# Optimization experiments

Hardware: AMD Instinct MI355X
Metric: run time of the kernel (lower is better)

The kernel has to match this reference:

```python
import jax, jax.numpy as jnp
import numpy as np

B, N = 4, 8192
MODEL_DIM, FEAT, HEADS, DIM, SIZE = 512, 64, 8, 3, 32
BN_EPS = 1e-5


def setup_inputs() -> dict:
    key = jax.random.key(0)
    ks = jax.random.split(key, 8)
    return {
        "input": jax.random.normal(ks[0], (B, MODEL_DIM, N), jnp.float32),
        "orig_pcd": jax.random.uniform(ks[1], (B, 3, N), jnp.float32, minval=-1.0, maxval=1.0),
        "conv_w": jax.random.normal(ks[2], (HEADS * (FEAT + 3), MODEL_DIM), jnp.float32) * (MODEL_DIM ** -0.5),
        "key_gamma": jax.random.normal(ks[3], (HEADS * 3,), jnp.float32) * 0.1,
        "key_beta": jnp.zeros((HEADS * 3,), jnp.float32),
        "val_gamma": jnp.ones((HEADS * FEAT,), jnp.float32),
        "val_beta": jnp.zeros((HEADS * FEAT,), jnp.float32),
        "proj": jax.random.normal(ks[4], (HEADS, DIM, 3), jnp.float32) * 0.5,
    }


def _bn(x, gamma, beta):
    # train-mode BatchNorm1d: normalize each channel over (batch, length); x: [B, C, N]
    mu = jnp.mean(x, axis=(0, 2), keepdims=True)
    var = jnp.var(x, axis=(0, 2), keepdims=True)
    xhat = (x - mu) * jax.lax.rsqrt(var + BN_EPS)
    return xhat * gamma[None, :, None] + beta[None, :, None]


def _splat(lattice, values):
    # lattice: [B, H, DIM, N] in (-1, 1); values: [B, H*FEAT, N]
    # DifferentiablePositions: map (-1,1) -> continuous grid coords in [0, SIZE-1]
    c = (lattice + 1.0) * 0.5 * (SIZE - 1)
    f = jnp.clip(jnp.floor(c), 0, SIZE - 2).astype(jnp.int32)   # base corner
    r = c - f.astype(c.dtype)                                    # local coord, [B,H,DIM,N]
    vals = values.reshape(B, HEADS, FEAT, N)
    data = jnp.moveaxis(vals, 2, -1)                             # [B,H,N,FEAT]
    strides = jnp.array([SIZE ** (DIM - 1 - d) for d in range(DIM)], jnp.int32)
    ncells = SIZE ** DIM
    bh = jnp.arange(B)[:, None] * HEADS + jnp.arange(HEADS)[None, :]  # [B,H]
    z = jnp.zeros((B * HEADS * ncells, FEAT), jnp.float32)
    # trilinear splat: scatter-add into the 2^DIM surrounding lattice cells
    for corner in range(2 ** DIM):
        bits = jnp.array([(corner >> (DIM - 1 - d)) & 1 for d in range(DIM)], jnp.int32)
        bits4 = bits[None, None, :, None]
        idx = f + bits4                                           # [B,H,DIM,N]
        w = jnp.prod(jnp.where(bits4 == 1, r, 1.0 - r), axis=2)   # [B,H,N]
        flat = jnp.sum(idx * strides[None, None, :, None], axis=2)  # [B,H,N]
        gid = (bh[:, :, None] * ncells + flat).reshape(-1)        # [B*H*N]
        z = z.at[gid].add((data * w[..., None]).reshape(-1, FEAT))
    return z.reshape(B, HEADS, ncells, FEAT).transpose(0, 1, 3, 2).reshape((B, HEADS, FEAT) + (SIZE,) * DIM)


def reference(input, orig_pcd, conv_w, key_gamma, key_beta, val_gamma, val_beta, proj):
    # 1x1 conv == channel GEMM: [B, H*(FEAT+3), N]
    kv = jnp.einsum('om,bmn->bon', conv_w, input)
    keys_res = _bn(kv[:, :HEADS * 3], key_gamma, key_beta)        # [B, H*3, N]
    values = _bn(kv[:, HEADS * 3:], val_gamma, val_beta)          # [B, H*FEAT, N]
    # per-head learned 3D->DIM projection of (pcd + predicted offset)
    pts = orig_pcd[:, None] + keys_res.reshape(B, HEADS, 3, N)    # [B,H,3,N]
    keys = jnp.einsum('hdk,bhkn->bhdn', proj, pts)                # [B,H,DIM,N]
    lattice = jnp.tanh(keys)
    z = _splat(lattice, values)                                   # [B,H,FEAT,S,S,S]
    occ = (jnp.abs(z) > 1e-9).sum().astype(jnp.float32) / (B * FEAT * HEADS)
    return z, occ, jnp.mean(keys), jnp.var(keys)
```

## Files before the change

kernel.cpp:

```cpp
#include <hip/hip_runtime.h>

#define B_     4
#define N_     8192
#define MD_    512
#define OC_    536
#define HEADS_ 8
#define FEAT_  64
#define NC_    32768
#define ZTOT_  67108864ll
#define NPTS_  262144
#define NKEYS_ 786432.0f
#define BNINV_ (1.0f / 32768.0f)

typedef __bf16 bf16x8 __attribute__((ext_vector_type(8)));
typedef float  f32x4  __attribute__((ext_vector_type(4)));

__device__ __forceinline__ unsigned short f2bf(float f) {
  unsigned int u = __float_as_uint(f);
  u = (u + 0x7FFFu + ((u >> 16) & 1u)) >> 16;
  return (unsigned short)u;
}
__device__ __forceinline__ float bf2f(unsigned short s) {
  return __uint_as_float(((unsigned)s) << 16);
}

__global__ __launch_bounds__(256) void convw_kernel(const float* __restrict__ W,
                                                    unsigned short* __restrict__ Wbf) {
  int i = (blockIdx.x * 256 + threadIdx.x) * 4;
  float4 v = *(const float4*)&W[24 * 512 + i];
  ushort4 o;
  o.x = f2bf(v.x); o.y = f2bf(v.y); o.z = f2bf(v.z); o.w = f2bf(v.w);
  *(ushort4*)&Wbf[i] = o;
}

__global__ __launch_bounds__(256) void convxt_kernel(const float* __restrict__ X,
                                                     unsigned short* __restrict__ Xt) {
  const int n0 = blockIdx.x * 64;
  const int k0 = blockIdx.y * 64;
  const int b  = blockIdx.z;
  __shared__ float T[64][65];
  const int t = threadIdx.x;
#pragma unroll
  for (int i = 0; i < 16; ++i) {
    int idx = t + i * 256;
    int kk = idx >> 6, nn = idx & 63;
    T[kk][nn] = X[((size_t)b * MD_ + k0 + kk) * N_ + n0 + nn];
  }
  __syncthreads();
  const int sub = t & 7;
  const int nb  = t >> 3;
#pragma unroll
  for (int i = 0; i < 2; ++i) {
    int nn = nb + i * 32;
    ushort4 o0, o1;
    o0.x = f2bf(T[sub * 8 + 0][nn]); o0.y = f2bf(T[sub * 8 + 1][nn]);
    o0.z = f2bf(T[sub * 8 + 2][nn]); o0.w = f2bf(T[sub * 8 + 3][nn]);
    o1.x = f2bf(T[sub * 8 + 4][nn]); o1.y = f2bf(T[sub * 8 + 5][nn]);
    o1.z = f2bf(T[sub * 8 + 6][nn]); o1.w = f2bf(T[sub * 8 + 7][nn]);
    unsigned short* dst = Xt + ((size_t)b * N_ + n0 + nn) * MD_ + k0 + sub * 8;
    *(ushort4*)dst = o0;
    *(ushort4*)(dst + 4) = o1;
  }
}

__global__ __launch_bounds__(256) void gemm_mfma(const unsigned short* __restrict__ Wbf,
                                                 const unsigned short* __restrict__ Xt,
                                                 const float* __restrict__ W,
                                                 const float* __restrict__ X,
                                                 unsigned short* __restrict__ valsbf,
                                                 float* __restrict__ kvk,
                                                 float* __restrict__ ssum,
                                                 float* __restrict__ s2sum) {
  __shared__ __align__(16) unsigned short smem[128 * 144];
  const int t = threadIdx.x;
  const int b = blockIdx.z;

  if (blockIdx.y == 4) {
    const int n0 = blockIdx.x * 128;
    float* Wt = (float*)smem;
    float* In = (float*)smem + 32 * 26;
    const int cg = t & 31;
    const int rb = (t >> 5) * 3;
    float acc[3][4];
#pragma unroll
    for (int r = 0; r < 3; ++r)
#pragma unroll
      for (int c = 0; c < 4; ++c) acc[r][c] = 0.f;
    const float* Xb = X + (size_t)b * MD_ * N_;
    for (int k0 = 0; k0 < MD_; k0 += 32) {
#pragma unroll
      for (int i = 0; i < 3; ++i) {
        int idx = t * 3 + i;
        int m = idx % 24, k = idx / 24;
        Wt[k * 26 + m] = W[(size_t)m * MD_ + k0 + k];
      }
#pragma unroll
      for (int i = 0; i < 4; ++i) {
        int slot = t + i * 256;
        int k = slot >> 5, n4 = slot & 31;
        float4 v = *(const float4*)(Xb + (size_t)(k0 + k) * N_ + n0 + n4 * 4);
        *(float4*)&In[k * 132 + n4 * 4] = v;
      }
      __syncthreads();
#pragma unroll
      for (int k = 0; k < 32; ++k) {
        float4 bv = *(const float4*)&In[k * 132 + cg * 4];
#pragma unroll
        for (int r = 0; r < 3; ++r) {
          float a = Wt[k * 26 + rb + r];
          acc[r][0] = fmaf(a, bv.x, acc[r][0]);
          acc[r][1] = fmaf(a, bv.y, acc[r][1]);
          acc[r][2] = fmaf(a, bv.z, acc[r][2]);
          acc[r][3] = fmaf(a, bv.w, acc[r][3]);
        }
      }
      __syncthreads();
    }
#pragma unroll
    for (int r = 0; r < 3; ++r) {
      float* dst = kvk + ((size_t)b * 24 + rb + r) * N_ + n0 + cg * 4;
      *(float4*)dst = *(float4*)&acc[r][0];
      float s = acc[r][0] + acc[r][1] + acc[r][2] + acc[r][3];
      float s2 = acc[r][0]*acc[r][0] + acc[r][1]*acc[r][1] +
                 acc[r][2]*acc[r][2] + acc[r][3]*acc[r][3];
#pragma unroll
      for (int off = 16; off; off >>= 1) {
        s  += __shfl_down(s, off, 32);
        s2 += __shfl_down(s2, off, 32);
      }
      if (cg == 0) { atomicAdd(&ssum[rb + r], s); atomicAdd(&s2sum[rb + r], s2); }
    }
    return;
  }

#define AL(r, c) smem[(r) * 72 + (c)]
#define BL(r, c) smem[128 * 72 + (r) * 72 + (c)]
#define CS(r, c) smem[(r) * 136 + (c)]
  const int n0 = blockIdx.x * 128;
  const int m0 = blockIdx.y * 128;
  const int lane = t & 63, wave = t >> 6;
  const int wm = wave >> 1, wn = wave & 1;
  f32x4 acc[4][4];
#pragma unroll
  for (int mi = 0; mi < 4; ++mi)
#pragma unroll
    for (int ni = 0; ni < 4; ++ni)
#pragma unroll
      for (int j = 0; j < 4; ++j) acc[mi][ni][j] = 0.f;

  const unsigned short* Xb = Xt + ((size_t)b * N_ + n0) * MD_;
  for (int k0 = 0; k0 < MD_; k0 += 64) {
#pragma unroll
    for (int i = 0; i < 4; ++i) {
      int chunk = t + i * 256;
      int r = chunk >> 3, c = chunk & 7;
      *(uint4*)&AL(r, c * 8) =
          *(const uint4*)&Wbf[(size_t)(m0 + r) * MD_ + k0 + c * 8];
    }
#pragma unroll
    for (int i = 0; i < 4; ++i) {
      int chunk = t + i * 256;
      int r = chunk >> 3, c = chunk & 7;
      *(uint4*)&BL(r, c * 8) =
          *(const uint4*)&Xb[(size_t)r * MD_ + k0 + c * 8];
    }
    __syncthreads();
#pragma unroll
    for (int ks = 0; ks < 2; ++ks) {
      bf16x8 af[4], bfr[4];
#pragma unroll
      for (int mi = 0; mi < 4; ++mi)
        af[mi] = *(const bf16x8*)&AL(wm * 64 + mi * 16 + (lane & 15),
                                     ks * 32 + (lane >> 4) * 8);
#pragma unroll
      for (int ni = 0; ni < 4; ++ni)
        bfr[ni] = *(const bf16x8*)&BL(wn * 64 + ni * 16 + (lane & 15),
                                      ks * 32 + (lane >> 4) * 8);
#pragma unroll
      for (int mi = 0; mi < 4; ++mi)
#pragma unroll
        for (int ni = 0; ni < 4; ++ni)
          acc[mi][ni] = __builtin_amdgcn_mfma_f32_16x16x32_bf16(
              af[mi], bfr[ni], acc[mi][ni], 0, 0, 0);
    }
    __syncthreads();
  }
#pragma unroll
  for (int mi = 0; mi < 4; ++mi)
#pragma unroll
    for (int j = 0; j < 4; ++j) {
      float s  = acc[mi][0][j] + acc[mi][1][j] + acc[mi][2][j] + acc[mi][3][j];
      float s2 = acc[mi][0][j]*acc[mi][0][j] + acc[mi][1][j]*acc[mi][1][j] +
                 acc[mi][2][j]*acc[mi][2][j] + acc[mi][3][j]*acc[mi][3][j];
#pragma unroll
      for (int off = 1; off < 16; off <<= 1) {
        s  += __shfl_xor(s, off);
        s2 += __shfl_xor(s2, off);
      }
      if ((lane & 15) == 0) {
        int mg = m0 + wm * 64 + mi * 16 + (lane >> 4) * 4 + j;
        atomicAdd(&ssum[24 + mg], s);
        atomicAdd(&s2sum[24 + mg], s2);
      }
    }
#pragma unroll
  for (int mi = 0; mi < 4; ++mi)
#pragma unroll
    for (int ni = 0; ni < 4; ++ni) {
      int row = wm * 64 + mi * 16 + (lane >> 4) * 4;
      int col = wn * 64 + ni * 16 + (lane & 15);
#pragma unroll
      for (int j = 0; j < 4; ++j)
        CS(row + j, col) = f2bf(acc[mi][ni][j]);
    }
  __syncthreads();
#pragma unroll
  for (int i = 0; i < 4; ++i) {
    int row = (t >> 3) + i * 32;
    int cb  = (t & 7) * 16;
    uint4 lo = *(const uint4*)&CS(row, cb);
    uint4 hi = *(const uint4*)&CS(row, cb + 8);
    unsigned short* dst = valsbf + ((size_t)b * 512 + m0 + row) * N_ + n0 + cb;
    *(uint4*)dst       = lo;
    *(uint4*)(dst + 8) = hi;
  }
#undef AL
#undef BL
#undef CS
}

__global__ __launch_bounds__(1024, 1) void sortk_kernel(const float* __restrict__ kvk,
                                                        const float* __restrict__ orig,
                                                        const float* __restrict__ proj,
                                                        const float* __restrict__ ssum,
                                                        const float* __restrict__ s2sum,
                                                        const float* __restrict__ kg,
                                                        const float* __restrict__ kb,
                                                        float4* __restrict__ sorted,
                                                        float* __restrict__ kacc) {
  const int bh = blockIdx.x;
  const int b = bh >> 3, h = bh & 7;
  __shared__ int hist[NC_];
  __shared__ int wsum[16];
  const int t = threadIdx.x;
  for (int i = t; i < NC_; i += 1024) hist[i] = 0;

  float sck[3], shk[3];
#pragma unroll
  for (int k = 0; k < 3; ++k) {
    int ch = h * 3 + k;
    float mu  = ssum[ch] * BNINV_;
    float var = s2sum[ch] * BNINV_ - mu * mu;
    sck[k] = kg[ch] * rsqrtf(var + 1e-5f);
    shk[k] = kb[ch] - mu * sck[k];
  }
  __syncthreads();

  const float* Kb = kvk + (size_t)b * 24 * N_;
  const float* Ob = orig + (size_t)b * 3 * N_;
  float4 mreg[8];
  float ksum = 0.f, ksq = 0.f;
#pragma unroll
  for (int i = 0; i < 8; ++i) {
    const int n = t + i * 1024;
    float pt[3];
#pragma unroll
    for (int k = 0; k < 3; ++k) {
      float kr = fmaf(Kb[(size_t)(h * 3 + k) * N_ + n], sck[k], shk[k]);
      pt[k] = Ob[(size_t)k * N_ + n] + kr;
    }
    int cell = 0;
    float rr[3];
#pragma unroll
    for (int d = 0; d < 3; ++d) {
      const float* pr = proj + (h * 3 + d) * 3;
      float key = pr[0] * pt[0] + pr[1] * pt[1] + pr[2] * pt[2];
      ksum += key; ksq += key * key;
      float lat = tanhf(key);
      float c = (lat + 1.0f) * 15.5f;
      float fl = floorf(c);
      fl = fminf(fmaxf(fl, 0.0f), 30.0f);
      rr[d] = c - fl;
      cell += (int)fl * ((d == 0) ? 1024 : (d == 1) ? 32 : 1);
    }
    mreg[i] = make_float4(rr[0], rr[1], rr[2], __int_as_float(cell | (n << 15)));
    atomicAdd(&hist[cell], 1);
  }
#pragma unroll
  for (int off = 32; off; off >>= 1) {
    ksum += __shfl_down(ksum, off);
    ksq  += __shfl_down(ksq, off);
  }
  if ((t & 63) == 0) {
    atomicAdd(&kacc[0], ksum);
    atomicAdd(&kacc[1], ksq);
  }
  __syncthreads();

  const int base = t * 32;
  int s = 0;
#pragma unroll
  for (int j = 0; j < 32; ++j) s += hist[base + ((j + t) & 31)];
  const int lane = t & 63, wv = t >> 6;
  int sc = s;
#pragma unroll
  for (int off = 1; off < 64; off <<= 1) {
    int x = __shfl_up(sc, off);
    if (lane >= off) sc += x;
  }
  if (lane == 63) wsum[wv] = sc;
  __syncthreads();
  if (t < 16) {
    int x = wsum[t];
    int sc2 = x;
#pragma unroll
    for (int off = 1; off < 16; off <<= 1) {
      int y = __shfl_up(sc2, off);
      if (t >= off) sc2 += y;
    }
    wsum[t] = sc2 - x;
  }
  __syncthreads();
  int run = sc - s + wsum[wv];
#pragma unroll
  for (int j = 0; j < 32; ++j) {
    int idx = base + ((j + t) & 31);
    int v = hist[idx];
    hist[idx] = run;
    run += v;
  }
  __syncthreads();
  float4* dst = sorted + (size_t)bh * N_;
#pragma unroll
  for (int i = 0; i < 8; ++i) {
    float4 m = mreg[i];
    int cell = __float_as_int(m.w) & 32767;
    int pos = atomicAdd(&hist[cell], 1);
    dst[pos] = m;
  }
}

__global__ __launch_bounds__(512, 1) void accum_kernel(const unsigned short* __restrict__ valsbf,
                                                       const float* __restrict__ ssum,
                                                       const float* __restrict__ s2sum,
                                                       const float* __restrict__ vg,
                                                       const float* __restrict__ vb,
                                                       const float4* __restrict__ sorted,
                                                       float* __restrict__ zout,
                                                       unsigned int* __restrict__ occ) {
  const int blk = blockIdx.x;
  const int f   = blk & 63;
  const int bh  = blk >> 6;
  const int b = bh >> 3, h = bh & 7;
  __shared__ float tile[NC_];
  __shared__ unsigned short kvs[N_];
  const int t = threadIdx.x;
#pragma unroll
  for (int i = 0; i < 16; ++i)
    ((float4*)tile)[t + i * 512] = make_float4(0.f, 0.f, 0.f, 0.f);
  const unsigned short* kvrow = valsbf + ((size_t)b * 512 + h * 64 + f) * N_;
  ((uint4*)kvs)[t]       = ((const uint4*)kvrow)[t];
  ((uint4*)kvs)[t + 512] = ((const uint4*)kvrow)[t + 512];
  __syncthreads();

  const int ch = 24 + h * 64 + f;
  const float mu  = ssum[ch] * BNINV_;
  const float var = s2sum[ch] * BNINV_ - mu * mu;
  const float sc  = vg[ch - 24] * rsqrtf(var + 1e-5f);
  const float sh  = vb[ch - 24] - mu * sc;
  const float4* sp = sorted + (size_t)bh * N_;
  const int base = t * 16;

  float4 e[16];
#pragma unroll
  for (int i = 0; i < 16; ++i) e[i] = sp[base + i];

#define FLUSH8()                                                    \
  {                                                                 \
    atomicAdd(&tile[cur],        m0_);                              \
    atomicAdd(&tile[cur + 1],    m1_);                              \
    atomicAdd(&tile[cur + 32],   m2_);                              \
    atomicAdd(&tile[cur + 33],   m3_);                              \
    atomicAdd(&tile[cur + 1024], m4_);                              \
    atomicAdd(&tile[cur + 1025], m5_);                              \
    atomicAdd(&tile[cur + 1056], m6_);                              \
    atomicAdd(&tile[cur + 1057], m7_);                              \
  }

  float m0_ = 0.f, m1_ = 0.f, m2_ = 0.f, m3_ = 0.f;
  float m4_ = 0.f, m5_ = 0.f, m6_ = 0.f, m7_ = 0.f;
  int cur = __float_as_int(e[0].w) & 32767;
#pragma unroll
  for (int i = 0; i < 16; ++i) {
    int packed = __float_as_int(e[i].w);
    int cell = packed & 32767;
    if (cell != cur) {
      if (cell == cur + 1) {
        atomicAdd(&tile[cur],        m0_);
        atomicAdd(&tile[cur + 32],   m2_);
        atomicAdd(&tile[cur + 1024], m4_);
        atomicAdd(&tile[cur + 1056], m6_);
        m0_ = m1_; m2_ = m3_; m4_ = m5_; m6_ = m7_;
        m1_ = 0.f; m3_ = 0.f; m5_ = 0.f; m7_ = 0.f;
      } else {
        FLUSH8();
        m0_ = m1_ = m2_ = m3_ = m4_ = m5_ = m6_ = m7_ = 0.f;
      }
      cur = cell;
    }
    float v  = fmaf(bf2f(kvs[(unsigned)packed >> 15]), sc, sh);
    float r0 = e[i].x, r1 = e[i].y, r2 = e[i].z;
    float va = v * (1.f - r0), vb2 = v * r0;
    float c00 = (1.f - r1) * (1.f - r2), c01 = (1.f - r1) * r2;
    float c10 = r1 * (1.f - r2),         c11 = r1 * r2;
    m0_ = fmaf(va, c00, m0_); m1_ = fmaf(va, c01, m1_);
    m2_ = fmaf(va, c10, m2_); m3_ = fmaf(va, c11, m3_);
    m4_ = fmaf(vb2, c00, m4_); m5_ = fmaf(vb2, c01, m5_);
    m6_ = fmaf(vb2, c10, m6_); m7_ = fmaf(vb2, c11, m7_);
  }
  FLUSH8();
#undef FLUSH8
  __syncthreads();

  unsigned int cnt = 0;
  float* dst = zout + (size_t)blk * NC_;
#pragma unroll
  for (int i = 0; i < 16; ++i) {
    float4 v = ((const float4*)tile)[t + i * 512];
    cnt += (fabsf(v.x) > 1e-9f) ? 1u : 0u;
    cnt += (fabsf(v.y) > 1e-9f) ? 1u : 0u;
    cnt += (fabsf(v.z) > 1e-9f) ? 1u : 0u;
    cnt += (fabsf(v.w) > 1e-9f) ? 1u : 0u;
    ((float4*)dst)[t + i * 512] = v;
  }
#pragma unroll
  for (int off = 32; off; off >>= 1) cnt += __shfl_down(cnt, off);
  __shared__ unsigned int wc[8];
  if ((t & 63) == 0) wc[t >> 6] = cnt;
  __syncthreads();
  if (t == 0) {
    unsigned int s = 0;
#pragma unroll
    for (int i = 0; i < 8; ++i) s += wc[i];
    atomicAdd(occ, s);
  }
}

__global__ __launch_bounds__(256) void gemm_full_kernel(const float* __restrict__ W,
                                                        const float* __restrict__ X,
                                                        float* __restrict__ KV) {
  const int n0 = blockIdx.x * 256;
  const int m0 = blockIdx.y * 64;
  const int b  = blockIdx.z;
  __shared__ float Wt[32][68];
  __shared__ float In[32][260];
  const int t  = threadIdx.x;
  const int tx = t & 31;
  const int ty = t >> 5;
  float acc[8][8];
#pragma unroll
  for (int r = 0; r < 8; ++r)
#pragma unroll
    for (int c = 0; c < 8; ++c) acc[r][c] = 0.f;
  const float* Xb = X + (size_t)b * MD_ * N_;
  for (int k0 = 0; k0 < MD_; k0 += 32) {
#pragma unroll
    for (int i = 0; i < 8; ++i) {
      int idx = t + i * 256;
      int m = idx >> 5, k = idx & 31;
      int mm = m0 + m;
      Wt[k][m] = (mm < OC_) ? W[(size_t)mm * MD_ + (k0 + k)] : 0.f;
    }
#pragma unroll
    for (int i = 0; i < 8; ++i) {
      int slot = t + i * 256;
      int k = slot >> 6, n4 = slot & 63;
      float4 v = *(const float4*)(Xb + (size_t)(k0 + k) * N_ + n0 + n4 * 4);
      *(float4*)&In[k][n4 * 4] = v;
    }
    __syncthreads();
#pragma unroll
    for (int k = 0; k < 32; ++k) {
      float a[8], bb[8];
      *(float4*)&a[0]  = *(const float4*)&Wt[k][ty * 8];
      *(float4*)&a[4]  = *(const float4*)&Wt[k][ty * 8 + 4];
      *(float4*)&bb[0] = *(const float4*)&In[k][tx * 4];
      *(float4*)&bb[4] = *(const float4*)&In[k][128 + tx * 4];
#pragma unroll
      for (int r = 0; r < 8; ++r)
#pragma unroll
        for (int c = 0; c < 8; ++c)
          acc[r][c] = fmaf(a[r], bb[c], acc[r][c]);
    }
    __syncthreads();
  }
#pragma unroll
  for (int r = 0; r < 8; ++r) {
    int mm = m0 + ty * 8 + r;
    if (mm < OC_) {
      float* dst = KV + ((size_t)b * OC_ + mm) * N_ + n0;
      *(float4*)(dst + tx * 4)       = *(float4*)&acc[r][0];
      *(float4*)(dst + 128 + tx * 4) = *(float4*)&acc[r][4];
    }
  }
}

__global__ __launch_bounds__(256) void bn_kernel(const float* __restrict__ KV,
                                                 const float* __restrict__ kg,
                                                 const float* __restrict__ kb,
                                                 const float* __restrict__ vg,
                                                 const float* __restrict__ vb,
                                                 float* __restrict__ scale,
                                                 float* __restrict__ shift) {
  const int o = blockIdx.x;
  const int t = threadIdx.x;
  float s = 0.f, s2 = 0.f;
  for (int idx = t; idx < B_ * N_; idx += 256) {
    int bb = idx >> 13, n = idx & (N_ - 1);
    float v = KV[((size_t)bb * OC_ + o) * N_ + n];
    s += v; s2 = fmaf(v, v, s2);
  }
#pragma unroll
  for (int off = 32; off; off >>= 1) {
    s  += __shfl_down(s, off);
    s2 += __shfl_down(s2, off);
  }
  __shared__ float rs[4], rs2[4];
  if ((t & 63) == 0) { rs[t >> 6] = s; rs2[t >> 6] = s2; }
  __syncthreads();
  if (t == 0) {
    s  = rs[0] + rs[1] + rs[2] + rs[3];
    s2 = rs2[0] + rs2[1] + rs2[2] + rs2[3];
    const float inv = 1.0f / (B_ * N_);
    float mu  = s * inv;
    float var = s2 * inv - mu * mu;
    float g, be;
    if (o < 24) { g = kg[o]; be = kb[o]; }
    else        { g = vg[o - 24]; be = vb[o - 24]; }
    float sc = g * rsqrtf(var + 1e-5f);
    scale[o] = sc;
    shift[o] = be - mu * sc;
  }
}

__global__ __launch_bounds__(256) void splat_final_kernel(const float* __restrict__ KV,
                                                          const float* __restrict__ orig,
                                                          const float* __restrict__ proj,
                                                          const float* __restrict__ scale,
                                                          const float* __restrict__ shift,
                                                          float* __restrict__ Z,
                                                          float* __restrict__ kacc) {
  const int bh = blockIdx.x >> 7;
  const int n0 = (blockIdx.x & 127) << 6;
  const int b = bh >> 3, h = bh & 7;
  __shared__ float vals[64][65];
  __shared__ int   cellS[64];
  __shared__ float rS[64][4];
  const int t = threadIdx.x;
  const float* KVb = KV + (size_t)b * OC_ * N_;
  const int ch0 = 24 + h * 64;
#pragma unroll
  for (int i = 0; i < 16; ++i) {
    int idx = t + i * 256;
    int f = idx >> 6, p = idx & 63;
    int ch = ch0 + f;
    vals[f][p] = fmaf(KVb[(size_t)ch * N_ + n0 + p], scale[ch], shift[ch]);
  }
  if (t < 64) {
    const int n = n0 + t;
    float pt[3];
#pragma unroll
    for (int k = 0; k < 3; ++k) {
      int ch = h * 3 + k;
      float kr = fmaf(KVb[(size_t)ch * N_ + n], scale[ch], shift[ch]);
      pt[k] = orig[((size_t)b * 3 + k) * N_ + n] + kr;
    }
    float ksum = 0.f, ksq = 0.f;
    int cell = 0;
    float rr[3];
#pragma unroll
    for (int d = 0; d < 3; ++d) {
      const float* pr = proj + (h * 3 + d) * 3;
      float key = pr[0] * pt[0] + pr[1] * pt[1] + pr[2] * pt[2];
      ksum += key; ksq += key * key;
      float lat = tanhf(key);
      float c = (lat + 1.0f) * 15.5f;
      float fl = floorf(c);
      fl = fminf(fmaxf(fl, 0.0f), 30.0f);
      rr[d] = c - fl;
      cell += (int)fl * ((d == 0) ? 1024 : (d == 1) ? 32 : 1);
    }
    cellS[t] = cell;
    rS[t][0] = rr[0]; rS[t][1] = rr[1]; rS[t][2] = rr[2];
#pragma unroll
    for (int off = 32; off; off >>= 1) {
      ksum += __shfl_down(ksum, off);
      ksq  += __shfl_down(ksq, off);
    }
    if (t == 0) { atomicAdd(&kacc[0], ksum); atomicAdd(&kacc[1], ksq); }
  }
  __syncthreads();
  const int w = t >> 6, l = t & 63;
  for (int pi = 0; pi < 16; ++pi) {
    int p = w * 16 + pi;
    int cell = cellS[p];
    float r0 = rS[p][0], r1 = rS[p][1], r2 = rS[p][2];
    float u0 = 1.f - r0, u1 = 1.f - r1, u2 = 1.f - r2;
    float v = vals[l][p];
#pragma unroll
    for (int c = 0; c < 8; ++c) {
      float wt = ((c & 4) ? r0 : u0) * ((c & 2) ? r1 : u1) * ((c & 1) ? r2 : u2);
      int cc = cell + ((c & 4) ? 1024 : 0) + ((c & 2) ? 32 : 0) + (c & 1);
      atomicAdd(Z + (size_t)(bh * 64 + l) * NC_ + cc, v * wt);
    }
  }
}

__global__ __launch_bounds__(256) void count_kernel(const float* __restrict__ Z,
                                                    unsigned int* __restrict__ occ) {
  unsigned int cnt = 0;
  for (long long i = (long long)blockIdx.x * blockDim.x + threadIdx.x; i < ZTOT_;
       i += (long long)gridDim.x * blockDim.x)
    cnt += (fabsf(Z[i]) > 1e-9f) ? 1u : 0u;
#pragma unroll
  for (int off = 32; off; off >>= 1) cnt += __shfl_down(cnt, off);
  __shared__ unsigned int wc[4];
  const int t = threadIdx.x;
  if ((t & 63) == 0) wc[t >> 6] = cnt;
  __syncthreads();
  if (t == 0) atomicAdd(occ, wc[0] + wc[1] + wc[2] + wc[3]);
}

__global__ void finalize_kernel(const unsigned int* __restrict__ occ,
                                const float* __restrict__ kacc,
                                float* __restrict__ tail) {
  float mean = kacc[0] / NKEYS_;
  tail[0] = (float)(*occ) * (1.0f / 2048.0f);
  tail[1] = mean;
  tail[2] = kacc[1] / NKEYS_ - mean * mean;
}

extern "C" void kernel_launch(void* const* d_in, const int* in_sizes, int n_in,
                              void* d_out, int out_size, void* d_ws, size_t ws_size,
                              hipStream_t stream) {
  const float* X    = (const float*)d_in[0];
  const float* orig = (const float*)d_in[1];
  const float* W    = (const float*)d_in[2];
  const float* kg   = (const float*)d_in[3];
  const float* kb   = (const float*)d_in[4];
  const float* vg   = (const float*)d_in[5];
  const float* vb   = (const float*)d_in[6];
  const float* proj = (const float*)d_in[7];
  float* out = (float*)d_out;

  float* P = (float*)d_ws;
  float* ssum  = P;
  float* s2sum = P + 544;
  float* kacc  = P + 1088;
  unsigned int* occ = (unsigned int*)(P + 1090);
  float* scale = P + 1152;
  float* shift = P + 1696;
  char* wsb = (char*)d_ws;

  const size_t need = (size_t)60 << 20;
  if (ws_size >= need) {
    unsigned short* Wbf    = (unsigned short*)(wsb + 65536);
    float*          kvk    = (float*)(wsb + ((size_t)1 << 20));
    float4*         sorted = (float4*)(wsb + ((size_t)5 << 20));
    unsigned short* valsbf = (unsigned short*)(wsb + ((size_t)9 << 20));
    unsigned short* Xt = (unsigned short*)out;

    hipMemsetAsync(P, 0, 4368, stream);

    convw_kernel<<<256, 256, 0, stream>>>(W, Wbf);
    convxt_kernel<<<dim3(128, 8, 4), 256, 0, stream>>>(X, Xt);
    gemm_mfma<<<dim3(64, 5, 4), 256, 0, stream>>>(Wbf, Xt, W, X,
                                                  valsbf, kvk, ssum, s2sum);
    sortk_kernel<<<32, 1024, 0, stream>>>(kvk, orig, proj, ssum, s2sum,
                                          kg, kb, sorted, kacc);
    accum_kernel<<<2048, 512, 0, stream>>>(valsbf, ssum, s2sum, vg, vb,
                                           sorted, out, occ);
    finalize_kernel<<<1, 1, 0, stream>>>(occ, kacc, out + ZTOT_);
  } else {
    float* kv = (float*)(wsb + 16384);
    hipMemsetAsync(P, 0, 4368, stream);
    hipMemsetAsync(out, 0, (size_t)ZTOT_ * 4, stream);
    gemm_full_kernel<<<dim3(N_ / 256, 9, B_), 256, 0, stream>>>(W, X, kv);
    bn_kernel<<<OC_, 256, 0, stream>>>(kv, kg, kb, vg, vb, scale, shift);
    splat_final_kernel<<<B_ * HEADS_ * (N_ / 64), 256, 0, stream>>>(
        kv, orig, proj, scale, shift, out, kacc);
    count_kernel<<<2048, 256, 0, stream>>>(out, occ);
    finalize_kernel<<<1, 1, 0, stream>>>(occ, kacc, out + ZTOT_);
  }
}
```

Baseline: 484.0 us.

## Split accum grid tile into four cell-range quarters to shrink LDS and raise occupancy

The accumulation kernel now splits each (batch, head, feature) grid tile into four quarters along the slowest axis, so each block holds an 8192-float LDS tile instead of 32768 and drops the one-block-per-CU launch bound. The sort kernel records, per quarter, the range of sorted points whose splats can touch that quarter, and each block walks only that range, clipping atomics to its quarter. The aim is to fit several blocks per CU and hide latency. In exchange, points near quarter borders are read and processed by two blocks, the launch has four times as many blocks, and the variable-length loop with bounds checks adds branching.

```diff
diff --git a/kernel.cpp b/kernel.cpp
--- a/kernel.cpp
+++ b/kernel.cpp
@@ -237,6 +237,8 @@
                                                         const float* __restrict__ kg,
                                                         const float* __restrict__ kb,
                                                         float4* __restrict__ sorted,
+                                                        int* __restrict__ qlo,
+                                                        int* __restrict__ qhi,
                                                         float* __restrict__ kacc) {
   const int bh = blockIdx.x;
   const int b = bh >> 3, h = bh & 7;
@@ -330,6 +332,11 @@
     run += v;
   }
   __syncthreads();
+  if (t < 4) {
+    qlo[bh * 4 + t] = (t == 0) ? 0 : hist[t * 8192 - 1057];
+    qhi[bh * 4 + t] = (t == 3) ? N_ : hist[(t + 1) * 8192];
+  }
+  __syncthreads();
   float4* dst = sorted + (size_t)bh * N_;
 #pragma unroll
   for (int i = 0; i < 8; ++i) {
@@ -340,23 +347,26 @@
   }
 }
 
-__global__ __launch_bounds__(512, 1) void accum_kernel(const unsigned short* __restrict__ valsbf,
-                                                       const float* __restrict__ ssum,
-                                                       const float* __restrict__ s2sum,
-                                                       const float* __restrict__ vg,
-                                                       const float* __restrict__ vb,
-                                                       const float4* __restrict__ sorted,
-                                                       float* __restrict__ zout,
-                                                       unsigned int* __restrict__ occ) {
+__global__ __launch_bounds__(512) void accum_kernel(const unsigned short* __restrict__ valsbf,
+                                                    const float* __restrict__ ssum,
+                                                    const float* __restrict__ s2sum,
+                                                    const float* __restrict__ vg,
+                                                    const float* __restrict__ vb,
+                                                    const float4* __restrict__ sorted,
+                                                    const int* __restrict__ qlo,
+                                                    const int* __restrict__ qhi,
+                                                    float* __restrict__ zout,
+                                                    unsigned int* __restrict__ occ) {
   const int blk = blockIdx.x;
-  const int f   = blk & 63;
-  const int bh  = blk >> 6;
+  const int q   = blk & 3;
+  const int f   = (blk >> 2) & 63;
+  const int bh  = blk >> 8;
   const int b = bh >> 3, h = bh & 7;
-  __shared__ float tile[NC_];
+  __shared__ float tile[8192];
   __shared__ unsigned short kvs[N_];
   const int t = threadIdx.x;
 #pragma unroll
-  for (int i = 0; i < 16; ++i)
+  for (int i = 0; i < 4; ++i)
     ((float4*)tile)[t + i * 512] = make_float4(0.f, 0.f, 0.f, 0.f);
   const unsigned short* kvrow = valsbf + ((size_t)b * 512 + h * 64 + f) * N_;
   ((uint4*)kvs)[t]       = ((const uint4*)kvrow)[t];
@@ -369,63 +379,78 @@
   const float sc  = vg[ch - 24] * rsqrtf(var + 1e-5f);
   const float sh  = vb[ch - 24] - mu * sc;
   const float4* sp = sorted + (size_t)bh * N_;
-  const int base = t * 16;
-
-  float4 e[16];
-#pragma unroll
-  for (int i = 0; i < 16; ++i) e[i] = sp[base + i];
-
-#define FLUSH8()                                                    \
-  {                                                                 \
-    atomicAdd(&tile[cur],        m0_);                              \
-    atomicAdd(&tile[cur + 1],    m1_);                              \
-    atomicAdd(&tile[cur + 32],   m2_);                              \
-    atomicAdd(&tile[cur + 33],   m3_);                              \
-    atomicAdd(&tile[cur + 1024], m4_);                              \
-    atomicAdd(&tile[cur + 1025], m5_);                              \
-    atomicAdd(&tile[cur + 1056], m6_);                              \
-    atomicAdd(&tile[cur + 1057], m7_);                              \
+  const int lo = q << 13;
+
+  const int e_lo = qlo[bh * 4 + q];
+  const int e_hi = qhi[bh * 4 + q];
+  const int count = e_hi - e_lo;
+  const int span = (count + 511) >> 9;
+  const int s0 = e_lo + t * span;
+  const int s1 = min(s0 + span, e_hi);
+
+#define FLUSH8() {                                                             \
+    int i0 = cur - lo;                                                         \
+    if ((unsigned)i0 < 8192u)          atomicAdd(&tile[i0],        m0_);       \
+    if ((unsigned)(i0 + 1) < 8192u)    atomicAdd(&tile[i0 + 1],    m1_);       \
+    if ((unsigned)(i0 + 32) < 8192u)   atomicAdd(&tile[i0 + 32],   m2_);       \
+    if ((unsigned)(i0 + 33) < 8192u)   atomicAdd(&tile[i0 + 33],   m3_);       \
+    if ((unsigned)(i0 + 1024) < 8192u) atomicAdd(&tile[i0 + 1024], m4_);       \
+    if ((unsigned)(i0 + 1025) < 8192u) atomicAdd(&tile[i0 + 1025], m5_);       \
+    if ((unsigned)(i0 + 1056) < 8192u) atomicAdd(&tile[i0 + 1056], m6_);       \
+    if ((unsigned)(i0 + 1057) < 8192u) atomicAdd(&tile[i0 + 1057], m7_);       \
   }
 
   float m0_ = 0.f, m1_ = 0.f, m2_ = 0.f, m3_ = 0.f;
   float m4_ = 0.f, m5_ = 0.f, m6_ = 0.f, m7_ = 0.f;
-  int cur = __float_as_int(e[0].w) & 32767;
-#pragma unroll
-  for (int i = 0; i < 16; ++i) {
-    int packed = __float_as_int(e[i].w);
-    int cell = packed & 32767;
-    if (cell != cur) {
-      if (cell == cur + 1) {
-        atomicAdd(&tile[cur],        m0_);
-        atomicAdd(&tile[cur + 32],   m2_);
-        atomicAdd(&tile[cur + 1024], m4_);
-        atomicAdd(&tile[cur + 1056], m6_);
-        m0_ = m1_; m2_ = m3_; m4_ = m5_; m6_ = m7_;
-        m1_ = 0.f; m3_ = 0.f; m5_ = 0.f; m7_ = 0.f;
-      } else {
-        FLUSH8();
-        m0_ = m1_ = m2_ = m3_ = m4_ = m5_ = m6_ = m7_ = 0.f;
+  int cur = -1;
+  for (int c0 = s0; c0 < s1; c0 += 8) {
+    float4 ee[8];
+#pragma unroll
+    for (int i = 0; i < 8; ++i) {
+      int idx = (c0 + i < s1) ? (c0 + i) : s0;
+      ee[i] = sp[idx];
+    }
+#pragma unroll
+    for (int i = 0; i < 8; ++i) {
+      bool live = (c0 + i) < s1;
+      int packed = __float_as_int(ee[i].w);
+      int cell = packed & 32767;
+      if (cell != cur) {
+        if (cur >= 0) {
+          if (cell == cur + 1) {
+            int i0 = cur - lo;
+            if ((unsigned)i0 < 8192u)          atomicAdd(&tile[i0],        m0_);
+            if ((unsigned)(i0 + 32) < 8192u)   atomicAdd(&tile[i0 + 32],   m2_);
+            if ((unsigned)(i0 + 1024) < 8192u) atomicAdd(&tile[i0 + 1024], m4_);
+            if ((unsigned)(i0 + 1056) < 8192u) atomicAdd(&tile[i0 + 1056], m6_);
+            m0_ = m1_; m2_ = m3_; m4_ = m5_; m6_ = m7_;
+            m1_ = 0.f; m3_ = 0.f; m5_ = 0.f; m7_ = 0.f;
+          } else {
+            FLUSH8();
+            m0_ = m1_ = m2_ = m3_ = m4_ = m5_ = m6_ = m7_ = 0.f;
+          }
+        }
+        cur = cell;
       }
-      cur = cell;
-    }
-    float v  = fmaf(bf2f(kvs[(unsigned)packed >> 15]), sc, sh);
-    float r0 = e[i].x, r1 = e[i].y, r2 = e[i].z;
-    float va = v * (1.f - r0), vb2 = v * r0;
-    float c00 = (1.f - r1) * (1.f - r2), c01 = (1.f - r1) * r2;
-    float c10 = r1 * (1.f - r2),         c11 = r1 * r2;
-    m0_ = fmaf(va, c00, m0_); m1_ = fmaf(va, c01, m1_);
-    m2_ = fmaf(va, c10, m2_); m3_ = fmaf(va, c11, m3_);
-    m4_ = fmaf(vb2, c00, m4_); m5_ = fmaf(vb2, c01, m5_);
-    m6_ = fmaf(vb2, c10, m6_); m7_ = fmaf(vb2, c11, m7_);
-  }
-  FLUSH8();
+      float v  = live ? fmaf(bf2f(kvs[(unsigned)packed >> 15]), sc, sh) : 0.f;
+      float r0 = ee[i].x, r1 = ee[i].y, r2 = ee[i].z;
+      float va = v * (1.f - r0), vb2 = v * r0;
+      float c00 = (1.f - r1) * (1.f - r2), c01 = (1.f - r1) * r2;
+      float c10 = r1 * (1.f - r2),         c11 = r1 * r2;
+      m0_ = fmaf(va, c00, m0_); m1_ = fmaf(va, c01, m1_);
+      m2_ = fmaf(va, c10, m2_); m3_ = fmaf(va, c11, m3_);
+      m4_ = fmaf(vb2, c00, m4_); m5_ = fmaf(vb2, c01, m5_);
+      m6_ = fmaf(vb2, c10, m6_); m7_ = fmaf(vb2, c11, m7_);
+    }
+  }
+  if (cur >= 0) FLUSH8();
 #undef FLUSH8
   __syncthreads();
 
   unsigned int cnt = 0;
-  float* dst = zout + (size_t)blk * NC_;
-#pragma unroll
-  for (int i = 0; i < 16; ++i) {
+  float* dst = zout + (((size_t)(bh * 64 + f)) << 15) + lo;
+#pragma unroll
+  for (int i = 0; i < 4; ++i) {
     float4 v = ((const float4*)tile)[t + i * 512];
     cnt += (fabsf(v.x) > 1e-9f) ? 1u : 0u;
     cnt += (fabsf(v.y) > 1e-9f) ? 1u : 0u;
@@ -666,6 +691,8 @@
   if (ws_size >= need) {
     unsigned short* Wbf    = (unsigned short*)(wsb + 65536);
     float*          kvk    = (float*)(wsb + ((size_t)1 << 20));
+    int*            qlo    = (int*)(wsb + ((size_t)4 << 20));
+    int*            qhi    = (int*)(wsb + ((size_t)4 << 20) + 4096);
     float4*         sorted = (float4*)(wsb + ((size_t)5 << 20));
     unsigned short* valsbf = (unsigned short*)(wsb + ((size_t)9 << 20));
     unsigned short* Xt = (unsigned short*)out;
@@ -677,9 +704,9 @@
     gemm_mfma<<<dim3(64, 5, 4), 256, 0, stream>>>(Wbf, Xt, W, X,
                                                   valsbf, kvk, ssum, s2sum);
     sortk_kernel<<<32, 1024, 0, stream>>>(kvk, orig, proj, ssum, s2sum,
-                                          kg, kb, sorted, kacc);
-    accum_kernel<<<2048, 512, 0, stream>>>(valsbf, ssum, s2sum, vg, vb,
-                                           sorted, out, occ);
+                                          kg, kb, sorted, qlo, qhi, kacc);
+    accum_kernel<<<32 * 256, 512, 0, stream>>>(valsbf, ssum, s2sum, vg, vb,
+                                               sorted, qlo, qhi, out, occ);
     finalize_kernel<<<1, 1, 0, stream>>>(occ, kacc, out + ZTOT_);
   } else {
     float* kv = (float*)(wsb + 16384);
```

After: 723.4 us. 1.49x slower.
